# Kernel tuning notes

Measured on AMD Instinct MI355X. Metric: run time of the kernel, lower is better.

The kernel has to match this reference:

```python
import jax, jax.numpy as jnp
import numpy as np

B, H, W, C = 2, 128, 128, 96
L = H * W
NUM_HEADS = 6
D_STATE = 16
DT_RANK = 6  # ceil(96/16)
D_CONV = 4
MLP_HIDDEN = 4 * C


def _layernorm(x, g, b, eps=1e-5):
    m = x.mean(-1, keepdims=True)
    v = x.var(-1, keepdims=True)
    return (x - m) * jax.lax.rsqrt(v + eps) * g + b


def _dwconv2d(x, w, b):
    # x: [B,C,H,W], w: [C,1,3,3] depthwise, padding=1 (torch 'same' for k=3)
    y = jax.lax.conv_general_dilated(x, w, (1, 1), [(1, 1), (1, 1)],
                                     dimension_numbers=('NCHW', 'OIHW', 'NCHW'),
                                     feature_group_count=x.shape[1])
    return y + b[None, :, None, None]


def _dwconv1d(x, w):
    # x: [B,C,L], w: [C,1,4]; torch padding='same' for even k=4 pads (1,2); bias is None (conv_bias//2 == 0)
    return jax.lax.conv_general_dilated(x, w, (1,), [(1, 2)],
                                        dimension_numbers=('NCH', 'OIH', 'NCH'),
                                        feature_group_count=x.shape[1])


def _rope(x):
    # x: [b, H, W, c]; 2D axial rotary embedding, k_max = c//4 per axis
    b, h, w, c = x.shape
    k_max = c // 4
    theta = 1.0 / (10000.0 ** (jnp.arange(k_max, dtype=jnp.float32) / k_max))
    ang_h = jnp.broadcast_to(jnp.arange(h, dtype=jnp.float32)[:, None, None] * theta, (h, w, k_max))
    ang_w = jnp.broadcast_to(jnp.arange(w, dtype=jnp.float32)[None, :, None] * theta, (h, w, k_max))
    angles = jnp.concatenate([ang_h, ang_w], -1)  # [h,w,c//2]
    cos, sin = jnp.cos(angles), jnp.sin(angles)
    xr, xi = x[..., 0::2], x[..., 1::2]  # consecutive pairs -> complex
    out_r = xr * cos - xi * sin
    out_i = xr * sin + xi * cos
    return jnp.stack([out_r, out_i], -1).reshape(x.shape)


def _linear_attention(x, qk_w, qk_b, lepe_w, lepe_b):
    # x: [b, n, c]
    b, n, c = x.shape
    hd = c // NUM_HEADS
    qk = x @ qk_w + qk_b  # [b,n,2c]
    q = jax.nn.elu(qk[..., :c]) + 1.0
    k = jax.nn.elu(qk[..., c:]) + 1.0
    v = x
    q_r = _rope(q.reshape(b, H, W, c)).reshape(b, n, NUM_HEADS, hd).transpose(0, 2, 1, 3)
    k_r = _rope(k.reshape(b, H, W, c)).reshape(b, n, NUM_HEADS, hd).transpose(0, 2, 1, 3)
    qh = q.reshape(b, n, NUM_HEADS, hd).transpose(0, 2, 1, 3)
    kh = k.reshape(b, n, NUM_HEADS, hd).transpose(0, 2, 1, 3)
    vh = v.reshape(b, n, NUM_HEADS, hd).transpose(0, 2, 1, 3)
    kmean = kh.mean(axis=2, keepdims=True)  # [b,h,1,hd]
    zden = 1.0 / (jnp.einsum('bhnd,bhmd->bhnm', qh, kmean) + 1e-6)  # [b,h,n,1]
    scale = n ** (-0.5)
    kv = jnp.einsum('bhnd,bhne->bhde', k_r * scale, vh * scale)  # [b,h,hd,hd]
    out = jnp.einsum('bhnd,bhde->bhne', q_r, kv) * zden
    out = out.transpose(0, 2, 1, 3).reshape(b, n, c)
    v2d = v.reshape(b, H, W, c).transpose(0, 3, 1, 2)
    lepe = _dwconv2d(v2d, lepe_w, lepe_b).transpose(0, 2, 3, 1).reshape(b, n, c)
    return out + lepe


def _selective_scan(u, delta, A, Bm, Cm, Dv):
    # u, delta: [b,d,l]; A: [d,n]; Bm, Cm: [b,n,l]; Dv: [d]
    dA = jnp.exp(jnp.einsum('bdl,dn->lbdn', delta, A))
    dBu = jnp.einsum('bdl,bnl,bdl->lbdn', delta, Bm, u)
    Ct = jnp.moveaxis(Cm, -1, 0)  # [l,b,n]

    def step(hcar, inp):
        dA_t, dBu_t, C_t = inp
        hcar = dA_t * hcar + dBu_t  # [b,d,n]
        y_t = jnp.einsum('bdn,bn->bd', hcar, C_t)
        return hcar, y_t

    h0 = jnp.zeros(dA.shape[1:], dtype=u.dtype)
    _, ys = jax.lax.scan(step, h0, (dA, dBu, Ct))  # ys: [l,b,d]
    y = jnp.moveaxis(ys, 0, -1)  # [b,d,l]
    return y + Dv[None, :, None] * u


def setup_inputs() -> dict:
    key = jax.random.key(0)
    ks = iter(jax.random.split(key, 40))

    def rn(shape, s=0.02):
        return jax.random.normal(next(ks), shape, jnp.float32) * s

    dt = jnp.exp(jax.random.uniform(next(ks), (C,), jnp.float32)
                 * (np.log(0.1) - np.log(0.001)) + np.log(0.001))
    dt_proj_b = dt + jnp.log(-jnp.expm1(-dt))
    return {
        'hidden_states': jax.random.normal(next(ks), (B, L, C), jnp.float32),
        'norm_in_g': jnp.ones((C,), jnp.float32),
        'norm_in_b': jnp.zeros((C,), jnp.float32),
        'in_proj_w': rn((C, 3 * C)),
        'dw_w': rn((C, 1, 3, 3)),
        'dw_b': rn((C,)),
        'qk_w': rn((C, 2 * C)),
        'qk_b': rn((2 * C,)),
        'lepe_w': rn((C, 1, 3, 3)),
        'lepe_b': rn((C,)),
        'conv_x_w': rn((C, 1, D_CONV)),
        'conv_z_w': rn((C, 1, D_CONV)),
        'x_proj_w': rn((C, DT_RANK + 2 * D_STATE)),
        'dt_proj_w': rn((DT_RANK, C), DT_RANK ** -0.5),
        'dt_proj_b': dt_proj_b,
        'A_log': jnp.log(jnp.broadcast_to(jnp.arange(1, D_STATE + 1, dtype=jnp.float32), (C, D_STATE)) + 0.0),
        'D': jnp.ones((C,), jnp.float32),
        'out_proj_w': rn((2 * C, C)),
        'proj_out_w': rn((C, C)),
        'proj_out_b': rn((C,)),
        'out_w': rn((2 * C, C)),
        'out_b': rn((C,)),
        'norm_mlp_g': jnp.ones((C,), jnp.float32),
        'norm_mlp_b': jnp.zeros((C,), jnp.float32),
        'fc1_w': rn((C, MLP_HIDDEN)),
        'fc1_b': rn((MLP_HIDDEN,)),
        'fc2_w': rn((MLP_HIDDEN, C)),
        'fc2_b': rn((C,)),
    }


def reference(hidden_states, norm_in_g, norm_in_b, in_proj_w, dw_w, dw_b, qk_w, qk_b,
              lepe_w, lepe_b, conv_x_w, conv_z_w, x_proj_w, dt_proj_w, dt_proj_b,
              A_log, D, out_proj_w, proj_out_w, proj_out_b, out_w, out_b,
              norm_mlp_g, norm_mlp_b, fc1_w, fc1_b, fc2_w, fc2_b):
    b, l, c = hidden_states.shape
    shortcut = hidden_states
    hs = _layernorm(hidden_states, norm_in_g, norm_in_b)
    xzw = jnp.transpose(hs @ in_proj_w, (0, 2, 1))  # [b,3c,l]
    x, z, w_ = jnp.split(xzw, 3, axis=1)  # each [b,c,l]
    # linear-attention branch
    lin_x = jax.nn.silu(_dwconv2d(w_.reshape(b, c, H, W), dw_w, dw_b))
    lin_x = jnp.transpose(lin_x, (0, 2, 3, 1)).reshape(b, l, c)
    lin_x = _linear_attention(lin_x, qk_w, qk_b, lepe_w, lepe_b)
    # selective-scan branch
    A = -jnp.exp(A_log)
    x = jax.nn.silu(_dwconv1d(x, conv_x_w))
    z = jax.nn.silu(_dwconv1d(z, conv_z_w))
    x_dbl = jnp.einsum('bdl,de->ble', x, x_proj_w)
    dt = x_dbl[..., :DT_RANK]
    Bm = jnp.transpose(x_dbl[..., DT_RANK:DT_RANK + D_STATE], (0, 2, 1))
    Cm = jnp.transpose(x_dbl[..., DT_RANK + D_STATE:], (0, 2, 1))
    delta = jax.nn.softplus(jnp.einsum('blr,rd->bdl', dt, dt_proj_w) + dt_proj_b[None, :, None])
    y = _selective_scan(x, delta, A, Bm, Cm, D)
    y = jnp.concatenate([y, z], axis=1)  # [b,2c,l]
    out1 = jnp.transpose(y, (0, 2, 1)) @ out_proj_w  # [b,l,c]
    z_t = jnp.transpose(z, (0, 2, 1))
    out2 = (lin_x * z_t) @ proj_out_w + proj_out_b
    out = jnp.concatenate([out1, out2], -1) @ out_w + out_b
    out = shortcut + out
    h2 = _layernorm(out, norm_mlp_g, norm_mlp_b)
    h2 = jax.nn.gelu(h2 @ fc1_w + fc1_b, approximate=False)
    return out + (h2 @ fc2_w + fc2_b)
```

## Files before the change

kernel.cpp:

```cpp
#include <hip/hip_runtime.h>
#include <hip/hip_bf16.h>
#include <math.h>

#define B_ 2
#define H_ 128
#define W_ 128
#define C_ 96
#define L_ (H_*W_)
#define BL_ (B_*L_)
#define NH_ 6
#define NPROJ_ 38
#define MLPH_ 384
#define NCH_ 512
#define CHL_ (L_/NCH_)
#define NG_ 32

typedef __attribute__((ext_vector_type(8))) short bf16x8;
typedef __attribute__((ext_vector_type(4))) float f32x4;
typedef __attribute__((ext_vector_type(4))) unsigned short us4v;

#define MFMA16(a,b,c) __builtin_amdgcn_mfma_f32_16x16x32_bf16(a,b,c,0,0,0)

#define WOFF1 0
#define WOFF2 54
#define WOFF3 90
#define WOFF4 126
#define WOFF5 144
#define WOFF6 180
#define WOFF7 252
#define WOFF8 324
#define WFRAGS 333

__device__ __forceinline__ float siluf(float x){ return x / (1.f + __expf(-x)); }
__device__ __forceinline__ unsigned short f2bf(float x){
    __hip_bfloat16 h = __float2bfloat16(x);
    return *reinterpret_cast<unsigned short*>(&h);
}
__device__ __forceinline__ unsigned pack2(float a, float b){
    return (unsigned)f2bf(a) | ((unsigned)f2bf(b) << 16);
}
__device__ __forceinline__ float bf2f(unsigned short u){
    return __uint_as_float((unsigned)u << 16);
}
__device__ __forceinline__ float gelu_fast(float x){
    float u_ = 0.7978845608f*x*(1.f + 0.044715f*x*x);
    float au = fabsf(u_);
    float e = __expf(-2.f*au);
    float th = (1.f - e)/(1.f + e);
    th = copysignf(th, u_);
    return 0.5f*x*(1.f + th);
}

__global__ __launch_bounds__(64) void k_setup(const float* __restrict__ w1,
    const float* __restrict__ w2, const float* __restrict__ w3,
    const float* __restrict__ w4, const float* __restrict__ w5,
    const float* __restrict__ w6, const float* __restrict__ w7,
    const float* __restrict__ dww, const float* __restrict__ lw,
    const float* __restrict__ xpw, const float* __restrict__ cxw,
    const float* __restrict__ czw,
    unsigned short* __restrict__ dst, float2* __restrict__ ctab,
    float* __restrict__ wt9, float* __restrict__ lw9, float* __restrict__ kvacc,
    float* __restrict__ wxT, float* __restrict__ wzT)
{
    int m = blockIdx.y;
    int l = threadIdx.x;
    if (m < 7){
        const float* srcs[7] = {w1,w2,w3,w4,w5,w6,w7};
        const int Ks[7]   = {96,96,192,96,192,96,384};
        const int Ns[7]   = {288,192,96,96,96,384,96};
        const int offs[7] = {WOFF1,WOFF2,WOFF3,WOFF4,WOFF5,WOFF6,WOFF7};
        int f = blockIdx.x;
        int nnt = Ns[m] >> 4, nkf = Ks[m] >> 5;
        if (f >= nnt*nkf) return;
        int kf = f / nnt, nt = f - kf*nnt;
        const float* s = srcs[m];
        unsigned short* d = dst + ((size_t)(offs[m] + f)*64 + l)*8;
        int krow = kf*32 + (l>>4)*8;
        int col  = nt*16 + (l&15);
        #pragma unroll
        for (int j=0;j<8;j++) d[j] = f2bf(s[(size_t)(krow+j)*Ns[m] + col]);
    } else {
        int x = blockIdx.x;
        if (x == 0){
            for (int i=l; i<128*24; i+=64){
                int pos = i/24, p = i%24;
                float th = powf(10000.f, -(float)p/24.f);
                float sn, cs; sincosf((float)pos*th, &sn, &cs);
                ctab[i] = make_float2(cs, sn);
            }
        } else if (x == 1){
            for (int i=l; i<3264; i+=64) kvacc[i] = 0.f;
        } else if (x == 2){
            for (int i=l; i<864; i+=64){
                int c = i/9, tap = i%9;
                wt9[tap*96 + c] = dww[i];
                lw9[tap*96 + c] = lw[i];
            }
        } else if (x == 3){
            for (int f=0; f<9; f++){
                int kf=f/3, nt=f%3;
                unsigned short* d = dst + ((size_t)(WOFF8 + f)*64 + l)*8;
                int krow = kf*32 + (l>>4)*8;
                int col  = nt*16 + (l&15);
                #pragma unroll
                for (int j=0;j<8;j++){
                    float v = (col < NPROJ_) ? xpw[(size_t)(krow+j)*NPROJ_ + col] : 0.f;
                    d[j] = f2bf(v);
                }
            }
        } else if (x == 4){
            for (int i=l; i<384; i+=64){
                int j = i/96, c = i%96;
                wxT[i] = cxw[c*4 + j];
                wzT[i] = czw[c*4 + j];
            }
        }
    }
}

__global__ __launch_bounds__(256) void k_ln_inproj_m(const float* __restrict__ hs,
    const float* __restrict__ gg, const float* __restrict__ bb,
    const unsigned short* __restrict__ wbf,
    unsigned short* __restrict__ xx, unsigned short* __restrict__ zz,
    unsigned short* __restrict__ ww)
{
    __shared__ unsigned short A[64*128];
    int t = threadIdx.x;
    size_t row0 = (size_t)blockIdx.x * 64;
    {
        int r = t >> 2, q = t & 3;
        const float* src = hs + (row0 + r)*C_ + q*24;
        float v[24];
        float s=0.f, s2=0.f;
        #pragma unroll
        for (int i=0;i<24;i++){ float x=src[i]; v[i]=x; s+=x; s2+=x*x; }
        s += __shfl_xor(s,1); s2 += __shfl_xor(s2,1);
        s += __shfl_xor(s,2); s2 += __shfl_xor(s2,2);
        float mn = s*(1.f/C_);
        float rs = rsqrtf(s2*(1.f/C_) - mn*mn + 1e-5f);
        int base = r*128, sw = (r&7)<<3;
        #pragma unroll
        for (int i=0;i<24;i+=2){
            int c = q*24 + i;
            float a0 = (v[i]  -mn)*rs*gg[c]   + bb[c];
            float a1 = (v[i+1]-mn)*rs*gg[c+1] + bb[c+1];
            *(unsigned*)&A[base + (c ^ sw)] = pack2(a0,a1);
        }
    }
    __syncthreads();
    int w = t>>6, l = t&63, lr = l&15, lh = l>>4;
    int arow = w*16 + lr;
    int abase = arow*128, asw = (arow&7)<<3;
    bf16x8 af[3];
    #pragma unroll
    for (int kf=0;kf<3;kf++)
        af[kf] = *(const bf16x8*)&A[abase + ((kf*32 + lh*8) ^ asw)];
    #pragma unroll 2
    for (int nt=0; nt<18; nt++){
        f32x4 acc = {0.f,0.f,0.f,0.f};
        #pragma unroll
        for (int kf=0;kf<3;kf++){
            bf16x8 bf_ = *(const bf16x8*)(wbf + ((size_t)((WOFF1 + kf*18 + nt)*64 + l))*8);
            acc = MFMA16(af[kf], bf_, acc);
        }
        unsigned short* base_;
        if (nt < 6) base_ = xx; else if (nt < 12) base_ = zz; else base_ = ww;
        int col = (nt%6)*16 + lr;
        unsigned short* dst = base_ + (row0 + w*16 + lh*4)*C_ + col;
        #pragma unroll
        for (int j=0;j<4;j++) dst[(size_t)j*C_] = f2bf(acc[j]);
    }
}

__global__ __launch_bounds__(256) void k_dwconv2d(const unsigned short* __restrict__ wwb,
    const float* __restrict__ wt9, const float* __restrict__ dwb,
    unsigned short* __restrict__ out)
{
    int gid = blockIdx.x*256 + threadIdx.x;
    int row = gid/24, c4 = gid%24; int c = c4*4;
    int b = row >> 14;
    int ll = row & (L_-1);
    int h = ll >> 7, wq = ll & 127;
    float a0=0.f,a1=0.f,a2=0.f,a3=0.f;
    #pragma unroll
    for (int kh=0; kh<3; kh++){
        int hh = h + kh - 1;
        if ((unsigned)hh < 128u){
            int base_row = (b<<14) + (hh<<7);
            #pragma unroll
            for (int kw=0; kw<3; kw++){
                int wp = wq + kw - 1;
                if ((unsigned)wp < 128u){
                    us4v v = *(const us4v*)&wwb[(size_t)(base_row + wp)*C_ + c];
                    float4 wt = *(const float4*)&wt9[(kh*3+kw)*96 + c];
                    a0 += bf2f(v[0])*wt.x; a1 += bf2f(v[1])*wt.y;
                    a2 += bf2f(v[2])*wt.z; a3 += bf2f(v[3])*wt.w;
                }
            }
        }
    }
    float4 bv = *(const float4*)&dwb[c];
    us4v o;
    o[0]=f2bf(siluf(a0+bv.x)); o[1]=f2bf(siluf(a1+bv.y));
    o[2]=f2bf(siluf(a2+bv.z)); o[3]=f2bf(siluf(a3+bv.w));
    *(us4v*)&out[(size_t)row*C_ + c] = o;
}

__global__ __launch_bounds__(256) void k_conv1d_xdbl(const unsigned short* __restrict__ xxb,
    const unsigned short* __restrict__ zzb, const float* __restrict__ wxT,
    const float* __restrict__ wzT, const unsigned short* __restrict__ wbf,
    const float* __restrict__ dtw, const float* __restrict__ dtb,
    float* __restrict__ xs, unsigned short* __restrict__ zb,
    float* __restrict__ delta, float* __restrict__ BC)
{
    __shared__ unsigned short A[64*128];
    __shared__ float XD[64][8];
    __shared__ float dtws[6][96];
    int t = threadIdx.x;
    size_t row0 = (size_t)blockIdx.x * 64;
    int b = (int)(row0 >> 14);
    int l0 = (int)(row0 & 16383);
    for (int i=t; i<576; i+=256) dtws[i/96][i%96] = dtw[i];
    for (int p=t; p<64*24; p+=256){
        int r = p/24, cq = p - r*24, c = cq*4;
        int l = l0 + r;
        float ax0=0.f,ax1=0.f,ax2=0.f,ax3=0.f;
        float az0=0.f,az1=0.f,az2=0.f,az3=0.f;
        #pragma unroll
        for (int j=0;j<4;j++){
            int lq = l - 1 + j;
            if ((unsigned)lq < (unsigned)L_){
                size_t off = ((size_t)(b<<14) + lq)*C_ + c;
                us4v xv = *(const us4v*)&xxb[off];
                us4v zv = *(const us4v*)&zzb[off];
                float4 wx4 = *(const float4*)&wxT[j*96 + c];
                float4 wz4 = *(const float4*)&wzT[j*96 + c];
                ax0 += bf2f(xv[0])*wx4.x; ax1 += bf2f(xv[1])*wx4.y;
                ax2 += bf2f(xv[2])*wx4.z; ax3 += bf2f(xv[3])*wx4.w;
                az0 += bf2f(zv[0])*wz4.x; az1 += bf2f(zv[1])*wz4.y;
                az2 += bf2f(zv[2])*wz4.z; az3 += bf2f(zv[3])*wz4.w;
            }
        }
        ax0=siluf(ax0); ax1=siluf(ax1); ax2=siluf(ax2); ax3=siluf(ax3);
        az0=siluf(az0); az1=siluf(az1); az2=siluf(az2); az3=siluf(az3);
        float4 xo={ax0,ax1,ax2,ax3};
        *(float4*)&xs[(row0+r)*C_ + c] = xo;
        us4v zo; zo[0]=f2bf(az0); zo[1]=f2bf(az1); zo[2]=f2bf(az2); zo[3]=f2bf(az3);
        *(us4v*)&zb[(row0+r)*C_ + c] = zo;
        int sw = (r&7)<<3;
        uint2 pk = { pack2(ax0,ax1), pack2(ax2,ax3) };
        *(uint2*)&A[r*128 + (c ^ sw)] = pk;
    }
    __syncthreads();
    int w=t>>6, l=t&63, lr=l&15, lh=l>>4;
    int arow = w*16+lr, asw=(arow&7)<<3;
    bf16x8 af[3];
    #pragma unroll
    for (int kf=0;kf<3;kf++)
        af[kf] = *(const bf16x8*)&A[arow*128 + ((kf*32 + lh*8) ^ asw)];
    #pragma unroll
    for (int nt=0; nt<3; nt++){
        f32x4 acc={0.f,0.f,0.f,0.f};
        #pragma unroll
        for (int kf=0;kf<3;kf++){
            bf16x8 bfr=*(const bf16x8*)(wbf + ((size_t)((WOFF8 + kf*3 + nt)*64 + l))*8);
            acc = MFMA16(af[kf], bfr, acc);
        }
        int col = nt*16 + lr;
        #pragma unroll
        for (int j=0;j<4;j++){
            int row = w*16 + lh*4 + j;
            if (col < 6) XD[row][col] = acc[j];
            else if (col < NPROJ_) BC[(row0+row)*32 + (col-6)] = acc[j];
        }
    }
    __syncthreads();
    {
        int r = t>>2, q = t&3;
        float xd0=XD[r][0], xd1=XD[r][1], xd2=XD[r][2];
        float xd3=XD[r][3], xd4=XD[r][4], xd5=XD[r][5];
        #pragma unroll
        for (int g=0; g<6; g++){
            int c = q*24 + g*4;
            float4 acc = *(const float4*)&dtb[c];
            float4 w0 = *(const float4*)&dtws[0][c];
            float4 w1 = *(const float4*)&dtws[1][c];
            float4 w2 = *(const float4*)&dtws[2][c];
            float4 w3 = *(const float4*)&dtws[3][c];
            float4 w4 = *(const float4*)&dtws[4][c];
            float4 w5 = *(const float4*)&dtws[5][c];
            acc.x += xd0*w0.x + xd1*w1.x + xd2*w2.x + xd3*w3.x + xd4*w4.x + xd5*w5.x;
            acc.y += xd0*w0.y + xd1*w1.y + xd2*w2.y + xd3*w3.y + xd4*w4.y + xd5*w5.y;
            acc.z += xd0*w0.z + xd1*w1.z + xd2*w2.z + xd3*w3.z + xd4*w4.z + xd5*w5.z;
            acc.w += xd0*w0.w + xd1*w1.w + xd2*w2.w + xd3*w3.w + xd4*w4.w + xd5*w5.w;
            float4 dl;
            dl.x = (acc.x>20.f)? acc.x : __logf(1.f+__expf(acc.x));
            dl.y = (acc.y>20.f)? acc.y : __logf(1.f+__expf(acc.y));
            dl.z = (acc.z>20.f)? acc.z : __logf(1.f+__expf(acc.z));
            dl.w = (acc.w>20.f)? acc.w : __logf(1.f+__expf(acc.w));
            *(float4*)&delta[(row0+r)*C_ + c] = dl;
        }
    }
}

__global__ __launch_bounds__(256) void k_qk_kv(const unsigned short* __restrict__ lin,
    const unsigned short* __restrict__ wbf, const float* __restrict__ qkb,
    const float2* __restrict__ ctab, unsigned short* __restrict__ qo,
    float* __restrict__ kvacc)
{
    __shared__ unsigned short A[64*128];
    __shared__ float KR[64*105];
    __shared__ float kmsum[96];
    int t = threadIdx.x;
    size_t row0 = (size_t)blockIdx.x * 64;
    int b = (int)(row0 >> 14);
    int l0 = (int)(row0 & 16383);
    for (int p = t; p < 64*12; p += 256){
        int r = p/12, c = (p - r*12)*8;
        int sw = (r&7)<<3;
        *(uint4*)&A[r*128 + (c ^ sw)] = *(const uint4*)&lin[(row0+r)*C_ + c];
    }
    if (t < 96) kmsum[t] = 0.f;
    __syncthreads();
    int w=t>>6, l=t&63, lr=l&15, lh=l>>4;
    int arow = w*16+lr; int asw=(arow&7)<<3;
    bf16x8 af[3];
    #pragma unroll
    for (int kf=0;kf<3;kf++)
        af[kf] = *(const bf16x8*)&A[arow*128 + ((kf*32 + lh*8) ^ asw)];
    #pragma unroll 2
    for (int nt=0; nt<12; nt++){
        f32x4 acc={0.f,0.f,0.f,0.f};
        #pragma unroll
        for (int kf=0;kf<3;kf++){
            bf16x8 bfr=*(const bf16x8*)(wbf + ((size_t)((WOFF2 + kf*12 + nt)*64 + l))*8);
            acc = MFMA16(af[kf], bfr, acc);
        }
        int colg = nt*16 + lr;
        float bias = qkb[colg];
        float vv[4];
        #pragma unroll
        for (int j=0;j<4;j++){
            float v = acc[j] + bias;
            vv[j] = (v>0.f)? v+1.f : __expf(v);
        }
        if (nt < 6){
            unsigned short* dp = qo + (row0 + w*16 + lh*4)*C_ + colg;
            #pragma unroll
            for (int j=0;j<4;j++) dp[(size_t)j*C_] = f2bf(vv[j]);
        } else {
            int ck = colg - 96;
            atomicAdd(&kmsum[ck], vv[0]+vv[1]+vv[2]+vv[3]);
            float pv[4];
            #pragma unroll
            for (int j=0;j<4;j++) pv[j] = __shfl_xor(vv[j], 1);
            int p = ck >> 1;
            #pragma unroll
            for (int j=0;j<4;j++){
                int rl = l0 + w*16 + lh*4 + j;
                int hp = rl>>7, wp = rl&127;
                float2 cssn = (p<24)? ctab[hp*24+p] : ctab[wp*24+(p-24)];
                float kr = (ck&1)? (pv[j]*cssn.y + vv[j]*cssn.x)
                                 : (vv[j]*cssn.x - pv[j]*cssn.y);
                KR[(w*16+lh*4+j)*105 + ck] = kr;
            }
        }
    }
    __syncthreads();
    for (int h = w; h < 6; h += 4){
        f32x4 acc = {0.f,0.f,0.f,0.f};
        #pragma unroll
        for (int kk=0; kk<2; kk++){
            union { bf16x8 v; unsigned short u[8]; } afu, bfu;
            #pragma unroll
            for (int j=0;j<8;j++){
                int rr = kk*32 + lh*8 + j;
                afu.u[j] = f2bf(KR[rr*105 + h*16 + lr]);
                bfu.u[j] = A[rr*128 + ((h*16+lr) ^ ((rr&7)<<3))];
            }
            acc = MFMA16(afu.v, bfu.v, acc);
        }
        #pragma unroll
        for (int i=0;i<4;i++)
            atomicAdd(&kvacc[b*1536 + h*256 + (lh*4+i)*16 + lr], acc[i]);
    }
    if (t < 96) atomicAdd(&kvacc[3072 + b*96 + t], kmsum[t]);
}

__global__ __launch_bounds__(384) void k_attnout(const unsigned short* __restrict__ qb,
    const unsigned short* __restrict__ vb, const unsigned short* __restrict__ zb,
    const float* __restrict__ kvacc, const float2* __restrict__ ctab,
    const float* __restrict__ lw9, const float* __restrict__ lb,
    unsigned short* __restrict__ azb)
{
    __shared__ float kvs[1536];
    __shared__ float kms[96];
    int t = threadIdx.x;
    size_t row0 = (size_t)blockIdx.x * 16;
    int b = (int)(row0 >> 14);
    const float invL = 1.f/16384.f;
    for (int i=t; i<1536; i+=384) kvs[i] = kvacc[b*1536+i]*invL;
    if (t < 96) kms[t] = kvacc[3072+b*96+t]*invL;
    __syncthreads();
    int r = t/24, c4 = t%24;
    int c = c4*4;
    int lrow = (int)(row0 & 16383) + r;
    int hp = lrow>>7, wp = lrow&127;
    size_t row = row0 + r;
    us4v qu = *(const us4v*)&qb[row*C_ + c];
    float q0=bf2f(qu[0]), q1=bf2f(qu[1]), q2=bf2f(qu[2]), q3=bf2f(qu[3]);
    int p0 = c>>1, p1 = p0+1;
    float2 cs0 = (p0<24)? ctab[hp*24+p0] : ctab[wp*24+(p0-24)];
    float2 cs1 = (p1<24)? ctab[hp*24+p1] : ctab[wp*24+(p1-24)];
    float4 qr;
    qr.x = q0*cs0.x - q1*cs0.y;
    qr.y = q0*cs0.y + q1*cs0.x;
    qr.z = q2*cs1.x - q3*cs1.y;
    qr.w = q2*cs1.y + q3*cs1.x;
    int h = c4>>2, j = c4&3;
    int dbase = j*4;
    float zp = q0*kms[h*16+dbase]   + q1*kms[h*16+dbase+1]
             + q2*kms[h*16+dbase+2] + q3*kms[h*16+dbase+3];
    zp += __shfl_xor(zp,1);
    zp += __shfl_xor(zp,2);
    float zd = 1.f/(zp + 1e-6f);
    float4 o = {0.f,0.f,0.f,0.f};
    #pragma unroll
    for (int g=0; g<4; g++){
        float4 qg;
        if (g==0) qg = qr;
        else {
            qg.x=__shfl_xor(qr.x,g); qg.y=__shfl_xor(qr.y,g);
            qg.z=__shfl_xor(qr.z,g); qg.w=__shfl_xor(qr.w,g);
        }
        int db = ((j^g)<<2);
        const float* kp = &kvs[h*256 + db*16 + j*4];
        #pragma unroll
        for (int i=0;i<4;i++){
            float qi = (i==0)?qg.x:(i==1)?qg.y:(i==2)?qg.z:qg.w;
            float4 kv4 = *(const float4*)&kp[i*16];
            o.x += qi*kv4.x; o.y += qi*kv4.y;
            o.z += qi*kv4.z; o.w += qi*kv4.w;
        }
    }
    float4 acc = *(const float4*)&lb[c];
    #pragma unroll
    for (int kh=0; kh<3; kh++){
        int hh = hp + kh - 1;
        if ((unsigned)hh < 128u){
            int base_row = (b<<14) + (hh<<7);
            #pragma unroll
            for (int kw=0; kw<3; kw++){
                int wq = wp + kw - 1;
                if ((unsigned)wq < 128u){
                    us4v v = *(const us4v*)&vb[(size_t)(base_row + wq)*C_ + c];
                    float4 wt = *(const float4*)&lw9[(kh*3+kw)*96 + c];
                    acc.x += bf2f(v[0])*wt.x; acc.y += bf2f(v[1])*wt.y;
                    acc.z += bf2f(v[2])*wt.z; acc.w += bf2f(v[3])*wt.w;
                }
            }
        }
    }
    us4v zu = *(const us4v*)&zb[row*C_ + c];
    us4v res;
    res[0] = f2bf((o.x*zd + acc.x)*bf2f(zu[0]));
    res[1] = f2bf((o.y*zd + acc.y)*bf2f(zu[1]));
    res[2] = f2bf((o.z*zd + acc.z)*bf2f(zu[2]));
    res[3] = f2bf((o.w*zd + acc.w)*bf2f(zu[3]));
    *(us4v*)&azb[row*C_ + c] = res;
}

__global__ __launch_bounds__(384) void k_scan1(const float* __restrict__ delta,
    const float* __restrict__ xs, const float* __restrict__ BC,
    const float* __restrict__ A_log, float* __restrict__ Ap, float* __restrict__ Be)
{
    int t = threadIdx.x; int nq = t&3, c = t>>2;
    int blk = blockIdx.x; int b = blk>>9, ch = blk&(NCH_-1);
    float4 a4 = *(const float4*)&A_log[c*16 + nq*4];
    float a0=-__expf(a4.x), a1=-__expf(a4.y), a2=-__expf(a4.z), a3=-__expf(a4.w);
    float ap0=1.f,ap1=1.f,ap2=1.f,ap3=1.f;
    float be0=0.f,be1=0.f,be2=0.f,be3=0.f;
    size_t base = ((size_t)b<<14) + ch*CHL_;
    for (int i=0;i<CHL_;i++){
        size_t row = base + i;
        float dl = delta[row*C_+c];
        float u  = xs[row*C_+c];
        float du = dl*u;
        float4 bc = *(const float4*)&BC[row*32 + nq*4];
        float e0=__expf(dl*a0), e1=__expf(dl*a1), e2=__expf(dl*a2), e3=__expf(dl*a3);
        ap0*=e0; be0=be0*e0+du*bc.x;
        ap1*=e1; be1=be1*e1+du*bc.y;
        ap2*=e2; be2=be2*e2+du*bc.z;
        ap3*=e3; be3=be3*e3+du*bc.w;
    }
    size_t o = (size_t)blk*1536 + c*16 + nq*4;
    float4 apv={ap0,ap1,ap2,ap3}, bev={be0,be1,be2,be3};
    *(float4*)&Ap[o] = apv;
    *(float4*)&Be[o] = bev;
}

__global__ __launch_bounds__(384) void k_scan2a(const float* __restrict__ Ap,
    const float* __restrict__ Be, float* __restrict__ GA, float* __restrict__ GB)
{
    int t = threadIdx.x; int blk = blockIdx.x;
    int b = blk>>5, g = blk&(NG_-1);
    int idx = (t>>2)*16 + (t&3)*4;
    float4 A = {1.f,1.f,1.f,1.f}, Bv = {0.f,0.f,0.f,0.f};
    for (int j=0;j<16;j++){
        size_t o = ((size_t)(b*NCH_ + g*16 + j))*1536 + idx;
        float4 a = *(const float4*)&Ap[o];
        float4 bb = *(const float4*)&Be[o];
        Bv.x=a.x*Bv.x+bb.x; Bv.y=a.y*Bv.y+bb.y; Bv.z=a.z*Bv.z+bb.z; Bv.w=a.w*Bv.w+bb.w;
        A.x*=a.x; A.y*=a.y; A.z*=a.z; A.w*=a.w;
    }
    size_t o = (size_t)blk*1536 + idx;
    *(float4*)&GA[o] = A;
    *(float4*)&GB[o] = Bv;
}

__global__ __launch_bounds__(256) void k_scan2b(const float* __restrict__ GA,
    const float* __restrict__ GB, float* __restrict__ Gin)
{
    int t = blockIdx.x*256 + threadIdx.x;
    int b = t/1536, m = t%1536;
    float h = 0.f;
    for (int g=0; g<NG_; g++){
        size_t o = ((size_t)(b*NG_+g))*1536 + m;
        Gin[o] = h;
        h = GA[o]*h + GB[o];
    }
}

__global__ __launch_bounds__(384) void k_scan2c(const float* __restrict__ Ap,
    const float* __restrict__ Be, const float* __restrict__ Gin,
    float* __restrict__ Hin)
{
    int t = threadIdx.x; int blk = blockIdx.x;
    int b = blk>>5, g = blk&(NG_-1);
    int idx = (t>>2)*16 + (t&3)*4;
    float4 h = *(const float4*)&Gin[(size_t)blk*1536 + idx];
    for (int j=0;j<16;j++){
        size_t o = ((size_t)(b*NCH_ + g*16 + j))*1536 + idx;
        *(float4*)&Hin[o] = h;
        float4 a = *(const float4*)&Ap[o];
        float4 bb = *(const float4*)&Be[o];
        h.x=a.x*h.x+bb.x; h.y=a.y*h.y+bb.y; h.z=a.z*h.z+bb.z; h.w=a.w*h.w+bb.w;
    }
}

__global__ __launch_bounds__(384) void k_scan3(const float* __restrict__ delta,
    const float* __restrict__ xs, const float* __restrict__ BC,
    const float* __restrict__ A_log, const float* __restrict__ Dv,
    const float* __restrict__ Hin, unsigned short* __restrict__ y)
{
    int t = threadIdx.x; int nq = t&3, c = t>>2;
    int blk = blockIdx.x; int b = blk>>9, ch = blk&(NCH_-1);
    float4 a4 = *(const float4*)&A_log[c*16 + nq*4];
    float a0=-__expf(a4.x), a1=-__expf(a4.y), a2=-__expf(a4.z), a3=-__expf(a4.w);
    float4 h = *(const float4*)&Hin[(size_t)blk*1536 + c*16 + nq*4];
    float Dc = Dv[c];
    size_t base = ((size_t)b<<14) + ch*CHL_;
    for (int i=0;i<CHL_;i++){
        size_t row = base + i;
        float dl = delta[row*C_+c];
        float u  = xs[row*C_+c];
        float du = dl*u;
        float4 bcB = *(const float4*)&BC[row*32 + nq*4];
        float4 bcC = *(const float4*)&BC[row*32 + 16 + nq*4];
        float e0=__expf(dl*a0), e1=__expf(dl*a1), e2=__expf(dl*a2), e3=__expf(dl*a3);
        h.x=h.x*e0+du*bcB.x; h.y=h.y*e1+du*bcB.y;
        h.z=h.z*e2+du*bcB.z; h.w=h.w*e3+du*bcB.w;
        float yv = h.x*bcC.x + h.y*bcC.y + h.z*bcC.z + h.w*bcC.w;
        yv += __shfl_xor(yv,1);
        yv += __shfl_xor(yv,2);
        if (nq == 0) y[row*C_+c] = f2bf(yv + Dc*u);
    }
}

__global__ __launch_bounds__(512) void k_combine_mlp(const unsigned short* __restrict__ yb,
    const unsigned short* __restrict__ zb, const unsigned short* __restrict__ azb,
    const unsigned short* __restrict__ wbf, const float* __restrict__ pob,
    const float* __restrict__ outb, const float* __restrict__ hs,
    const float* __restrict__ gg, const float* __restrict__ bb,
    const float* __restrict__ f1b, const float* __restrict__ f2b,
    float* __restrict__ outr)
{
    __shared__ __attribute__((aligned(16))) char POOL[65536];
    __shared__ float LNS[64][2], LNS2[64][2];
    unsigned short* C2 = (unsigned short*)POOL;
    unsigned short* AT = (unsigned short*)POOL;
    unsigned short* HID= (unsigned short*)(POOL + 16384);
    int t=threadIdx.x;
    size_t row0=(size_t)blockIdx.x*64;
    int w=t>>6, l=t&63, lr=l&15, lh=l>>4;
    int rt=w>>1, hf=w&1;
    int arow=rt*16+lr; int asw=(arow&7)<<3;
    size_t gbase = (row0+arow)*C_;
    bf16x8 af1[6], af2[3];
    #pragma unroll
    for (int kf=0;kf<3;kf++){
        af1[kf]   = *(const bf16x8*)&yb[gbase + kf*32 + lh*8];
        af1[3+kf] = *(const bf16x8*)&zb[gbase + kf*32 + lh*8];
        af2[kf]   = *(const bf16x8*)&azb[gbase + kf*32 + lh*8];
    }
    #pragma unroll
    for (int q=0;q<3;q++){
        int nt = hf*3 + q;
        f32x4 a1={0.f,0.f,0.f,0.f}, a2={0.f,0.f,0.f,0.f};
        #pragma unroll
        for (int kf=0;kf<6;kf++){
            bf16x8 b=*(const bf16x8*)(wbf+((size_t)((WOFF3+kf*6+nt)*64+l))*8);
            a1=MFMA16(af1[kf],b,a1);
        }
        #pragma unroll
        for (int kf=0;kf<3;kf++){
            bf16x8 b=*(const bf16x8*)(wbf+((size_t)((WOFF4+kf*6+nt)*64+l))*8);
            a2=MFMA16(af2[kf],b,a2);
        }
        int col=nt*16+lr;
        float pb=pob[col];
        #pragma unroll
        for (int j=0;j<4;j++){
            int row=rt*16+lh*4+j;
            int sw2=(row&7)<<3;
            C2[row*192 + (col^sw2)] = f2bf(a1[j]);
            C2[row*192 + ((96+col)^sw2)] = f2bf(a2[j]+pb);
        }
    }
    __syncthreads();
    bf16x8 af3[6];
    #pragma unroll
    for (int kf=0;kf<6;kf++) af3[kf]=*(const bf16x8*)&C2[arow*192 + ((kf*32+lh*8)^asw)];
    float outv[3][4];
    #pragma unroll
    for (int q=0;q<3;q++){
        int nt = hf*3 + q;
        f32x4 acc={0.f,0.f,0.f,0.f};
        #pragma unroll
        for (int kf=0;kf<6;kf++){
            bf16x8 b=*(const bf16x8*)(wbf+((size_t)((WOFF5+kf*6+nt)*64+l))*8);
            acc=MFMA16(af3[kf],b,acc);
        }
        int col=nt*16+lr;
        float ob=outb[col];
        #pragma unroll
        for (int j=0;j<4;j++){
            size_t row=row0+rt*16+lh*4+j;
            outv[q][j] = acc[j] + ob + hs[row*C_+col];
        }
    }
    float s_[4], s2_[4];
    #pragma unroll
    for (int j=0;j<4;j++){
        float s=0.f, s2=0.f;
        #pragma unroll
        for (int q=0;q<3;q++){ float v=outv[q][j]; s+=v; s2+=v*v; }
        s_[j]=s; s2_[j]=s2;
    }
    #pragma unroll
    for (int m=1;m<16;m<<=1){
        #pragma unroll
        for (int j=0;j<4;j++){
            s_[j]  += __shfl_xor(s_[j],  m);
            s2_[j] += __shfl_xor(s2_[j], m);
        }
    }
    if (lr==0){
        #pragma unroll
        for (int j=0;j<4;j++){
            int row = rt*16+lh*4+j;
            LNS[row][hf]  = s_[j];
            LNS2[row][hf] = s2_[j];
        }
    }
    __syncthreads();
    #pragma unroll
    for (int j=0;j<4;j++){
        int row = rt*16+lh*4+j;
        float s  = LNS[row][0]  + LNS[row][1];
        float s2 = LNS2[row][0] + LNS2[row][1];
        float mn = s*(1.f/C_);
        float rs = rsqrtf(s2*(1.f/C_) - mn*mn + 1e-5f);
        int sw2 = (row&7)<<3;
        #pragma unroll
        for (int q=0;q<3;q++){
            int col = (hf*3+q)*16+lr;
            AT[row*128 + (col^sw2)] = f2bf((outv[q][j]-mn)*rs*gg[col]+bb[col]);
        }
    }
    __syncthreads();
    {
        bf16x8 af[3];
        #pragma unroll
        for(int kf=0;kf<3;kf++) af[kf]=*(const bf16x8*)&AT[arow*128+((kf*32+lh*8)^asw)];
        #pragma unroll 2
        for(int q=0;q<12;q++){
            int nt = hf*12 + q;
            f32x4 acc={0.f,0.f,0.f,0.f};
            #pragma unroll
            for(int kf=0;kf<3;kf++){
                bf16x8 b=*(const bf16x8*)(wbf+((size_t)((WOFF6+kf*24+nt)*64+l))*8);
                acc=MFMA16(af[kf],b,acc);
            }
            int col=nt*16+lr;
            float bias=f1b[col];
            #pragma unroll
            for(int j=0;j<4;j++){
                int row=rt*16+lh*4+j;
                HID[row*384 + (col^((row&7)<<3))] = f2bf(gelu_fast(acc[j]+bias));
            }
        }
    }
    __syncthreads();
    {
        bf16x8 afh[12];
        #pragma unroll
        for(int kf=0;kf<12;kf++) afh[kf]=*(const bf16x8*)&HID[arow*384+((kf*32+lh*8)^asw)];
        #pragma unroll
        for(int q=0;q<3;q++){
            int nt = hf*3 + q;
            f32x4 acc={0.f,0.f,0.f,0.f};
            #pragma unroll
            for(int kf=0;kf<12;kf++){
                bf16x8 b=*(const bf16x8*)(wbf+((size_t)((WOFF7+kf*6+nt)*64+l))*8);
                acc=MFMA16(afh[kf],b,acc);
            }
            int col=nt*16+lr;
            float bias=f2b[col];
            #pragma unroll
            for(int j=0;j<4;j++){
                size_t row=row0+rt*16+lh*4+j;
                outr[row*C_+col] = outv[q][j] + acc[j] + bias;
            }
        }
    }
}

extern "C" void kernel_launch(void* const* d_in, const int* in_sizes, int n_in,
                              void* d_out, int out_size, void* d_ws, size_t ws_size,
                              hipStream_t stream)
{
    const float* hs        = (const float*)d_in[0];
    const float* norm_in_g = (const float*)d_in[1];
    const float* norm_in_b = (const float*)d_in[2];
    const float* in_proj_w = (const float*)d_in[3];
    const float* dw_w      = (const float*)d_in[4];
    const float* dw_b      = (const float*)d_in[5];
    const float* qk_w      = (const float*)d_in[6];
    const float* qk_b      = (const float*)d_in[7];
    const float* lepe_w    = (const float*)d_in[8];
    const float* lepe_b    = (const float*)d_in[9];
    const float* conv_x_w  = (const float*)d_in[10];
    const float* conv_z_w  = (const float*)d_in[11];
    const float* x_proj_w  = (const float*)d_in[12];
    const float* dt_proj_w = (const float*)d_in[13];
    const float* dt_proj_b = (const float*)d_in[14];
    const float* A_log     = (const float*)d_in[15];
    const float* Dv        = (const float*)d_in[16];
    const float* out_proj_w= (const float*)d_in[17];
    const float* proj_out_w= (const float*)d_in[18];
    const float* proj_out_b= (const float*)d_in[19];
    const float* out_w     = (const float*)d_in[20];
    const float* out_b     = (const float*)d_in[21];
    const float* norm_mlp_g= (const float*)d_in[22];
    const float* norm_mlp_b= (const float*)d_in[23];
    const float* fc1_w     = (const float*)d_in[24];
    const float* fc1_b     = (const float*)d_in[25];
    const float* fc2_w     = (const float*)d_in[26];
    const float* fc2_b     = (const float*)d_in[27];

    float* ws = (float*)d_ws;
    size_t o = 0;
    const size_t USH = (size_t)BL_*C_/2;
    unsigned short* xxb  = (unsigned short*)(ws + o); o += USH;
    unsigned short* zzb  = (unsigned short*)(ws + o); o += USH;
    unsigned short* wwb  = (unsigned short*)(ws + o); o += USH;
    unsigned short* linb = (unsigned short*)(ws + o); o += USH;
    unsigned short* zbuf = (unsigned short*)(ws + o); o += USH;
    float* xs    = ws + o; o += (size_t)BL_*C_;
    float* delta = ws + o; o += (size_t)BL_*C_;
    float* BC    = ws + o; o += (size_t)BL_*32;
    float* Ap    = ws + o; o += (size_t)B_*NCH_*1536;
    float* Be    = ws + o; o += (size_t)B_*NCH_*1536;
    float* Hin   = ws + o; o += (size_t)B_*NCH_*1536;
    float* GA    = ws + o; o += (size_t)B_*NG_*1536;
    float* GB    = ws + o; o += (size_t)B_*NG_*1536;
    float* Gin   = ws + o; o += (size_t)B_*NG_*1536;
    float* kvacc = ws + o; o += 3264;
    float2* ctab = (float2*)(ws + o); o += 6144;
    float* wt9   = ws + o; o += 864;
    float* lw9   = ws + o; o += 864;
    float* wxT   = ws + o; o += 384;
    float* wzT   = ws + o; o += 384;
    unsigned short* wbf = (unsigned short*)(ws + o);

    unsigned short* qb  = xxb;
    unsigned short* yb  = zzb;
    unsigned short* azb = wwb;
    float* outr = (float*)d_out;

    k_setup<<<dim3(72,8), 64, 0, stream>>>(in_proj_w, qk_w, out_proj_w, proj_out_w,
                                           out_w, fc1_w, fc2_w, dw_w, lepe_w,
                                           x_proj_w, conv_x_w, conv_z_w,
                                           wbf, ctab, wt9, lw9, kvacc, wxT, wzT);
    k_ln_inproj_m<<<BL_/64, 256, 0, stream>>>(hs, norm_in_g, norm_in_b, wbf,
                                              xxb, zzb, wwb);
    k_dwconv2d<<<(BL_*24)/256, 256, 0, stream>>>(wwb, wt9, dw_b, linb);
    k_conv1d_xdbl<<<BL_/64, 256, 0, stream>>>(xxb, zzb, wxT, wzT, wbf,
                                              dt_proj_w, dt_proj_b, xs, zbuf, delta, BC);
    k_qk_kv<<<BL_/64, 256, 0, stream>>>(linb, wbf, qk_b, ctab, qb, kvacc);
    k_attnout<<<BL_/16, 384, 0, stream>>>(qb, linb, zbuf, kvacc, ctab, lw9, lepe_b, azb);
    k_scan1<<<B_*NCH_, 384, 0, stream>>>(delta, xs, BC, A_log, Ap, Be);
    k_scan2a<<<B_*NG_, 384, 0, stream>>>(Ap, Be, GA, GB);
    k_scan2b<<<12, 256, 0, stream>>>(GA, GB, Gin);
    k_scan2c<<<B_*NG_, 384, 0, stream>>>(Ap, Be, Gin, Hin);
    k_scan3<<<B_*NCH_, 384, 0, stream>>>(delta, xs, BC, A_log, Dv, Hin, yb);
    k_combine_mlp<<<BL_/64, 512, 0, stream>>>(yb, zbuf, azb, wbf, proj_out_b,
                                              out_b, hs, norm_mlp_g, norm_mlp_b,
                                              fc1_b, fc2_b, outr);
}
```

Before: 191.8 us.

## Fuse scan chunk-summary pass into conv1d/xproj kernel and store delta, x in half precision

Folds the first chunk-scan pass (k_scan1) into k_conv1d_xdbl, which now computes the per-chunk decay products and state contributions from delta, x and B kept in shared memory. That removes one kernel launch and a full reread of delta, xs and BC. Delta is now stored as fp16 and xs as bf16 instead of fp32, which halves the traffic in k_scan3. The block grows to 384 threads with more shared memory, which may reduce occupancy, and the lower-precision delta and x in the second scan pass may shift numerics.

Measured after the change: 185.5 us. 3.3% less time.

```diff
diff --git a/kernel.cpp b/kernel.cpp
--- a/kernel.cpp
+++ b/kernel.cpp
@@ -1,5 +1,6 @@
 #include <hip/hip_runtime.h>
 #include <hip/hip_bf16.h>
+#include <hip/hip_fp16.h>
 #include <math.h>
 
 #define B_ 2
@@ -41,6 +42,14 @@
 }
 __device__ __forceinline__ float bf2f(unsigned short u){
     return __uint_as_float((unsigned)u << 16);
+}
+__device__ __forceinline__ unsigned short f2h(float x){
+    __half h = __float2half(x);
+    return *reinterpret_cast<unsigned short*>(&h);
+}
+__device__ __forceinline__ float h2f(unsigned short u){
+    __half h = *reinterpret_cast<__half*>(&u);
+    return __half2float(h);
 }
 __device__ __forceinline__ float gelu_fast(float x){
     float u_ = 0.7978845608f*x*(1.f + 0.044715f*x*x);
@@ -206,22 +215,26 @@
     *(us4v*)&out[(size_t)row*C_ + c] = o;
 }
 
-__global__ __launch_bounds__(256) void k_conv1d_xdbl(const unsigned short* __restrict__ xxb,
+__global__ __launch_bounds__(384) void k_conv1d_xdbl(const unsigned short* __restrict__ xxb,
     const unsigned short* __restrict__ zzb, const float* __restrict__ wxT,
     const float* __restrict__ wzT, const unsigned short* __restrict__ wbf,
     const float* __restrict__ dtw, const float* __restrict__ dtb,
-    float* __restrict__ xs, unsigned short* __restrict__ zb,
-    float* __restrict__ delta, float* __restrict__ BC)
+    const float* __restrict__ A_log,
+    unsigned short* __restrict__ xsb, unsigned short* __restrict__ zb,
+    unsigned short* __restrict__ dlh, float* __restrict__ BC,
+    float* __restrict__ Ap, float* __restrict__ Be)
 {
     __shared__ unsigned short A[64*128];
     __shared__ float XD[64][8];
     __shared__ float dtws[6][96];
+    __shared__ float sdl[64][96];
+    __shared__ float sbc[64][32];
     int t = threadIdx.x;
     size_t row0 = (size_t)blockIdx.x * 64;
     int b = (int)(row0 >> 14);
     int l0 = (int)(row0 & 16383);
-    for (int i=t; i<576; i+=256) dtws[i/96][i%96] = dtw[i];
-    for (int p=t; p<64*24; p+=256){
+    for (int i=t; i<576; i+=384) dtws[i/96][i%96] = dtw[i];
+    for (int p=t; p<64*24; p+=384){
         int r = p/24, cq = p - r*24, c = cq*4;
         int l = l0 + r;
         float ax0=0.f,ax1=0.f,ax2=0.f,ax3=0.f;
@@ -243,39 +256,43 @@
         }
         ax0=siluf(ax0); ax1=siluf(ax1); ax2=siluf(ax2); ax3=siluf(ax3);
         az0=siluf(az0); az1=siluf(az1); az2=siluf(az2); az3=siluf(az3);
-        float4 xo={ax0,ax1,ax2,ax3};
-        *(float4*)&xs[(row0+r)*C_ + c] = xo;
+        us4v xo; xo[0]=f2bf(ax0); xo[1]=f2bf(ax1); xo[2]=f2bf(ax2); xo[3]=f2bf(ax3);
+        *(us4v*)&xsb[(row0+r)*C_ + c] = xo;
         us4v zo; zo[0]=f2bf(az0); zo[1]=f2bf(az1); zo[2]=f2bf(az2); zo[3]=f2bf(az3);
         *(us4v*)&zb[(row0+r)*C_ + c] = zo;
         int sw = (r&7)<<3;
-        uint2 pk = { pack2(ax0,ax1), pack2(ax2,ax3) };
-        *(uint2*)&A[r*128 + (c ^ sw)] = pk;
+        *(us4v*)&A[r*128 + (c ^ sw)] = xo;
     }
     __syncthreads();
     int w=t>>6, l=t&63, lr=l&15, lh=l>>4;
-    int arow = w*16+lr, asw=(arow&7)<<3;
-    bf16x8 af[3];
-    #pragma unroll
-    for (int kf=0;kf<3;kf++)
-        af[kf] = *(const bf16x8*)&A[arow*128 + ((kf*32 + lh*8) ^ asw)];
-    #pragma unroll
-    for (int nt=0; nt<3; nt++){
-        f32x4 acc={0.f,0.f,0.f,0.f};
-        #pragma unroll
-        for (int kf=0;kf<3;kf++){
-            bf16x8 bfr=*(const bf16x8*)(wbf + ((size_t)((WOFF8 + kf*3 + nt)*64 + l))*8);
-            acc = MFMA16(af[kf], bfr, acc);
-        }
-        int col = nt*16 + lr;
-        #pragma unroll
-        for (int j=0;j<4;j++){
-            int row = w*16 + lh*4 + j;
-            if (col < 6) XD[row][col] = acc[j];
-            else if (col < NPROJ_) BC[(row0+row)*32 + (col-6)] = acc[j];
-        }
-    }
-    __syncthreads();
-    {
+    if (w < 4){
+        int arow = w*16+lr, asw=(arow&7)<<3;
+        bf16x8 af[3];
+        #pragma unroll
+        for (int kf=0;kf<3;kf++)
+            af[kf] = *(const bf16x8*)&A[arow*128 + ((kf*32 + lh*8) ^ asw)];
+        #pragma unroll
+        for (int nt=0; nt<3; nt++){
+            f32x4 acc={0.f,0.f,0.f,0.f};
+            #pragma unroll
+            for (int kf=0;kf<3;kf++){
+                bf16x8 bfr=*(const bf16x8*)(wbf + ((size_t)((WOFF8 + kf*3 + nt)*64 + l))*8);
+                acc = MFMA16(af[kf], bfr, acc);
+            }
+            int col = nt*16 + lr;
+            #pragma unroll
+            for (int j=0;j<4;j++){
+                int row = w*16 + lh*4 + j;
+                if (col < 6) XD[row][col] = acc[j];
+                else if (col < NPROJ_){
+                    BC[(row0+row)*32 + (col-6)] = acc[j];
+                    sbc[row][col-6] = acc[j];
+                }
+            }
+        }
+    }
+    __syncthreads();
+    if (t < 256){
         int r = t>>2, q = t&3;
         float xd0=XD[r][0], xd1=XD[r][1], xd2=XD[r][2];
         float xd3=XD[r][3], xd4=XD[r][4], xd5=XD[r][5];
@@ -298,7 +315,38 @@
             dl.y = (acc.y>20.f)? acc.y : __logf(1.f+__expf(acc.y));
             dl.z = (acc.z>20.f)? acc.z : __logf(1.f+__expf(acc.z));
             dl.w = (acc.w>20.f)? acc.w : __logf(1.f+__expf(acc.w));
-            *(float4*)&delta[(row0+r)*C_ + c] = dl;
+            sdl[r][c]=dl.x; sdl[r][c+1]=dl.y; sdl[r][c+2]=dl.z; sdl[r][c+3]=dl.w;
+            us4v dh; dh[0]=f2h(dl.x); dh[1]=f2h(dl.y); dh[2]=f2h(dl.z); dh[3]=f2h(dl.w);
+            *(us4v*)&dlh[(row0+r)*C_ + c] = dh;
+        }
+    }
+    __syncthreads();
+    {
+        int c = t>>2, nq = t&3;
+        float4 a4 = *(const float4*)&A_log[c*16 + nq*4];
+        float a0=-__expf(a4.x), a1=-__expf(a4.y), a2=-__expf(a4.z), a3=-__expf(a4.w);
+        int chbase = b*NCH_ + (l0>>5);
+        int csw_c = c;
+        #pragma unroll
+        for (int chunk=0; chunk<2; chunk++){
+            float ap0=1.f,ap1=1.f,ap2=1.f,ap3=1.f;
+            float be0=0.f,be1=0.f,be2=0.f,be3=0.f;
+            for (int i=0;i<CHL_;i++){
+                int row = chunk*CHL_ + i;
+                float dl = sdl[row][c];
+                float u = bf2f(A[row*128 + (csw_c ^ ((row&7)<<3))]);
+                float du = dl*u;
+                float4 bc = *(const float4*)&sbc[row][nq*4];
+                float e0=__expf(dl*a0), e1=__expf(dl*a1), e2=__expf(dl*a2), e3=__expf(dl*a3);
+                ap0*=e0; be0=be0*e0+du*bc.x;
+                ap1*=e1; be1=be1*e1+du*bc.y;
+                ap2*=e2; be2=be2*e2+du*bc.z;
+                ap3*=e3; be3=be3*e3+du*bc.w;
+            }
+            size_t o = (size_t)(chbase+chunk)*1536 + c*16 + nq*4;
+            float4 apv={ap0,ap1,ap2,ap3}, bev={be0,be1,be2,be3};
+            *(float4*)&Ap[o] = apv;
+            *(float4*)&Be[o] = bev;
         }
     }
 }
@@ -470,35 +518,6 @@
     *(us4v*)&azb[row*C_ + c] = res;
 }
 
-__global__ __launch_bounds__(384) void k_scan1(const float* __restrict__ delta,
-    const float* __restrict__ xs, const float* __restrict__ BC,
-    const float* __restrict__ A_log, float* __restrict__ Ap, float* __restrict__ Be)
-{
-    int t = threadIdx.x; int nq = t&3, c = t>>2;
-    int blk = blockIdx.x; int b = blk>>9, ch = blk&(NCH_-1);
-    float4 a4 = *(const float4*)&A_log[c*16 + nq*4];
-    float a0=-__expf(a4.x), a1=-__expf(a4.y), a2=-__expf(a4.z), a3=-__expf(a4.w);
-    float ap0=1.f,ap1=1.f,ap2=1.f,ap3=1.f;
-    float be0=0.f,be1=0.f,be2=0.f,be3=0.f;
-    size_t base = ((size_t)b<<14) + ch*CHL_;
-    for (int i=0;i<CHL_;i++){
-        size_t row = base + i;
-        float dl = delta[row*C_+c];
-        float u  = xs[row*C_+c];
-        float du = dl*u;
-        float4 bc = *(const float4*)&BC[row*32 + nq*4];
-        float e0=__expf(dl*a0), e1=__expf(dl*a1), e2=__expf(dl*a2), e3=__expf(dl*a3);
-        ap0*=e0; be0=be0*e0+du*bc.x;
-        ap1*=e1; be1=be1*e1+du*bc.y;
-        ap2*=e2; be2=be2*e2+du*bc.z;
-        ap3*=e3; be3=be3*e3+du*bc.w;
-    }
-    size_t o = (size_t)blk*1536 + c*16 + nq*4;
-    float4 apv={ap0,ap1,ap2,ap3}, bev={be0,be1,be2,be3};
-    *(float4*)&Ap[o] = apv;
-    *(float4*)&Be[o] = bev;
-}
-
 __global__ __launch_bounds__(384) void k_scan2a(const float* __restrict__ Ap,
     const float* __restrict__ Be, float* __restrict__ GA, float* __restrict__ GB)
 {
@@ -548,8 +567,8 @@
     }
 }
 
-__global__ __launch_bounds__(384) void k_scan3(const float* __restrict__ delta,
-    const float* __restrict__ xs, const float* __restrict__ BC,
+__global__ __launch_bounds__(384) void k_scan3(const unsigned short* __restrict__ dlh,
+    const unsigned short* __restrict__ xsb, const float* __restrict__ BC,
     const float* __restrict__ A_log, const float* __restrict__ Dv,
     const float* __restrict__ Hin, unsigned short* __restrict__ y)
 {
@@ -562,8 +581,8 @@
     size_t base = ((size_t)b<<14) + ch*CHL_;
     for (int i=0;i<CHL_;i++){
         size_t row = base + i;
-        float dl = delta[row*C_+c];
-        float u  = xs[row*C_+c];
+        float dl = h2f(dlh[row*C_+c]);
+        float u  = bf2f(xsb[row*C_+c]);
         float du = dl*u;
         float4 bcB = *(const float4*)&BC[row*32 + nq*4];
         float4 bcC = *(const float4*)&BC[row*32 + 16 + nq*4];
@@ -777,8 +796,8 @@
     unsigned short* wwb  = (unsigned short*)(ws + o); o += USH;
     unsigned short* linb = (unsigned short*)(ws + o); o += USH;
     unsigned short* zbuf = (unsigned short*)(ws + o); o += USH;
-    float* xs    = ws + o; o += (size_t)BL_*C_;
-    float* delta = ws + o; o += (size_t)BL_*C_;
+    unsigned short* xsb  = (unsigned short*)(ws + o); o += USH;
+    unsigned short* dlh  = (unsigned short*)(ws + o); o += USH;
     float* BC    = ws + o; o += (size_t)BL_*32;
     float* Ap    = ws + o; o += (size_t)B_*NCH_*1536;
     float* Be    = ws + o; o += (size_t)B_*NCH_*1536;
@@ -806,15 +825,15 @@
     k_ln_inproj_m<<<BL_/64, 256, 0, stream>>>(hs, norm_in_g, norm_in_b, wbf,
                                               xxb, zzb, wwb);
     k_dwconv2d<<<(BL_*24)/256, 256, 0, stream>>>(wwb, wt9, dw_b, linb);
-    k_conv1d_xdbl<<<BL_/64, 256, 0, stream>>>(xxb, zzb, wxT, wzT, wbf,
-                                              dt_proj_w, dt_proj_b, xs, zbuf, delta, BC);
+    k_conv1d_xdbl<<<BL_/64, 384, 0, stream>>>(xxb, zzb, wxT, wzT, wbf,
+                                              dt_proj_w, dt_proj_b, A_log,
+                                              xsb, zbuf, dlh, BC, Ap, Be);
     k_qk_kv<<<BL_/64, 256, 0, stream>>>(linb, wbf, qk_b, ctab, qb, kvacc);
     k_attnout<<<BL_/16, 384, 0, stream>>>(qb, linb, zbuf, kvacc, ctab, lw9, lepe_b, azb);
-    k_scan1<<<B_*NCH_, 384, 0, stream>>>(delta, xs, BC, A_log, Ap, Be);
     k_scan2a<<<B_*NG_, 384, 0, stream>>>(Ap, Be, GA, GB);
     k_scan2b<<<12, 256, 0, stream>>>(GA, GB, Gin);
     k_scan2c<<<B_*NG_, 384, 0, stream>>>(Ap, Be, Gin, Hin);
-    k_scan3<<<B_*NCH_, 384, 0, stream>>>(delta, xs, BC, A_log, Dv, Hin, yb);
+    k_scan3<<<B_*NCH_, 384, 0, stream>>>(dlh, xsb, BC, A_log, Dv, Hin, yb);
     k_combine_mlp<<<BL_/64, 512, 0, stream>>>(yb, zbuf, azb, wbf, proj_out_b,
                                               out_b, hs, norm_mlp_g, norm_mlp_b,
                                               fc1_b, fc2_b, outr);
```
